# Performance work log

Measured on AMD Instinct MI355X. Metric: run time of the kernel, lower is better.

## Reference

```python
import jax, jax.numpy as jnp
import numpy as np

N_ENT = 500000
N_REL = 1000
EMB = 256
B = 65536
EPS = 1e-12


def setup_inputs() -> dict:
    key = jax.random.key(0)
    ks = jax.random.split(key, 7)
    all_emb = jax.random.normal(ks[0], (N_ENT + N_REL, EMB), dtype=jnp.float32)
    pos_h = jax.random.randint(ks[1], (B,), 0, N_ENT)
    pos_r = jax.random.randint(ks[2], (B,), 0, N_REL)
    pos_t = jax.random.randint(ks[3], (B,), 0, N_ENT)
    neg_h = jax.random.randint(ks[4], (B,), 0, N_ENT)
    neg_r = jax.random.randint(ks[5], (B,), 0, N_REL)
    neg_t = jax.random.randint(ks[6], (B,), 0, N_ENT)
    return {"all_emb": all_emb, "pos_h": pos_h, "pos_r": pos_r, "pos_t": pos_t,
            "neg_h": neg_h, "neg_r": neg_r, "neg_t": neg_t, "n_ent": N_ENT}


def reference(all_emb, pos_h, pos_r, pos_t, neg_h, neg_r, neg_t, n_ent):
    # forward() first L2-normalizes entity rows in-place (normalize_entity_weights)
    ent = all_emb[:n_ent]
    nrm = jnp.maximum(jnp.linalg.norm(ent, axis=1, keepdims=True), EPS)
    emb = jnp.concatenate([ent / nrm, all_emb[n_ent:]], axis=0)

    # sparse.mm(adj, emb) with rows (+1@h, +1@(n_ent+r), -1@t) == gather-combine
    def score(h, r, t):
        v = emb[h] + emb[r + n_ent] - emb[t]          # [B, EMB]
        return -jnp.sum(v * v, axis=1)                 # -||.||_2^2, [B]

    pos_calc = score(pos_h, pos_r, pos_t)
    neg_calc = score(neg_h, neg_r, neg_t)
    return (pos_calc, neg_calc)
```

## Files before the change

### kernel.cpp

```cpp
#include <hip/hip_runtime.h>


#define EMB 256
#define EPS 1e-12f
#define SPW 4

__global__ __launch_bounds__(256) void transe_score_diag2x_kernel(
    const float* __restrict__ emb,
    const int* __restrict__ pos_h, const int* __restrict__ pos_r, const int* __restrict__ pos_t,
    const int* __restrict__ neg_h, const int* __restrict__ neg_r, const int* __restrict__ neg_t,
    const int* __restrict__ n_ent_ptr,
    float* __restrict__ out, int B)
{
    const int wave = (blockIdx.x * blockDim.x + threadIdx.x) >> 6;
    const int lane = threadIdx.x & 63;
    const int base = wave * SPW;
    if (base >= 2 * B) return;

    const int n_ent = *n_ent_ptr;

    const int* __restrict__ hsrc;
    const int* __restrict__ rsrc;
    const int* __restrict__ tsrc;
    int off;
    if (base < B) { hsrc = pos_h; rsrc = pos_r; tsrc = pos_t; off = base; }
    else          { hsrc = neg_h; rsrc = neg_r; tsrc = neg_t; off = base - B; }

    const int4 hh = *(const int4*)(hsrc + off);
    const int4 rr = *(const int4*)(rsrc + off);
    const int4 tt = *(const int4*)(tsrc + off);

    const int hi[SPW] = {hh.x, hh.y, hh.z, hh.w};
    const int ri[SPW] = {rr.x, rr.y, rr.z, rr.w};
    const int ti[SPW] = {tt.x, tt.y, tt.z, tt.w};

    {
        float4 hv[SPW], tv[SPW], rv[SPW];
#pragma unroll
        for (int s = 0; s < SPW; ++s) {
            hv[s] = ((const float4*)(emb + (size_t)hi[s] * EMB))[lane];
            tv[s] = ((const float4*)(emb + (size_t)ti[s] * EMB))[lane];
            rv[s] = ((const float4*)(emb + ((size_t)ri[s] + (size_t)n_ent) * EMB))[lane];
        }

        float red[2 * SPW];
#pragma unroll
        for (int s = 0; s < SPW; ++s) {
            red[s]       = hv[s].x * hv[s].x + hv[s].y * hv[s].y + hv[s].z * hv[s].z + hv[s].w * hv[s].w;
            red[SPW + s] = tv[s].x * tv[s].x + tv[s].y * tv[s].y + tv[s].z * tv[s].z + tv[s].w * tv[s].w;
        }
#pragma unroll
        for (int d = 32; d >= 1; d >>= 1) {
#pragma unroll
            for (int k = 0; k < 2 * SPW; ++k)
                red[k] += __shfl_xor(red[k], d, 64);
        }

        float sq[SPW];
#pragma unroll
        for (int s = 0; s < SPW; ++s) {
            const float inh = 1.0f / fmaxf(sqrtf(red[s]), EPS);
            const float itn = 1.0f / fmaxf(sqrtf(red[SPW + s]), EPS);
            const float vx = hv[s].x * inh + rv[s].x - tv[s].x * itn;
            const float vy = hv[s].y * inh + rv[s].y - tv[s].y * itn;
            const float vz = hv[s].z * inh + rv[s].z - tv[s].z * itn;
            const float vw = hv[s].w * inh + rv[s].w - tv[s].w * itn;
            sq[s] = vx * vx + vy * vy + vz * vz + vw * vw;
        }
#pragma unroll
        for (int d = 32; d >= 1; d >>= 1) {
#pragma unroll
            for (int k = 0; k < SPW; ++k)
                sq[k] += __shfl_xor(sq[k], d, 64);
        }

        if (lane == 0)
            *(float4*)(out + base) = make_float4(-sq[0], -sq[1], -sq[2], -sq[3]);
    }

    __builtin_amdgcn_sched_barrier(0);

    unsigned long long p = (unsigned long long)(const void*)emb;
    asm volatile("" : "+s"(p));
    const float* emb2 = (const float*)p;

    {
        float4 hv[SPW], tv[SPW], rv[SPW];
#pragma unroll
        for (int s = 0; s < SPW; ++s) {
            hv[s] = ((const float4*)(emb2 + (size_t)hi[s] * EMB))[lane];
            tv[s] = ((const float4*)(emb2 + (size_t)ti[s] * EMB))[lane];
            rv[s] = ((const float4*)(emb2 + ((size_t)ri[s] + (size_t)n_ent) * EMB))[lane];
        }

        float red[2 * SPW];
#pragma unroll
        for (int s = 0; s < SPW; ++s) {
            red[s]       = hv[s].x * hv[s].x + hv[s].y * hv[s].y + hv[s].z * hv[s].z + hv[s].w * hv[s].w;
            red[SPW + s] = tv[s].x * tv[s].x + tv[s].y * tv[s].y + tv[s].z * tv[s].z + tv[s].w * tv[s].w;
        }
#pragma unroll
        for (int d = 32; d >= 1; d >>= 1) {
#pragma unroll
            for (int k = 0; k < 2 * SPW; ++k)
                red[k] += __shfl_xor(red[k], d, 64);
        }

        float sq[SPW];
#pragma unroll
        for (int s = 0; s < SPW; ++s) {
            const float inh = 1.0f / fmaxf(sqrtf(red[s]), EPS);
            const float itn = 1.0f / fmaxf(sqrtf(red[SPW + s]), EPS);
            const float vx = hv[s].x * inh + rv[s].x - tv[s].x * itn;
            const float vy = hv[s].y * inh + rv[s].y - tv[s].y * itn;
            const float vz = hv[s].z * inh + rv[s].z - tv[s].z * itn;
            const float vw = hv[s].w * inh + rv[s].w - tv[s].w * itn;
            sq[s] = vx * vx + vy * vy + vz * vz + vw * vw;
        }
#pragma unroll
        for (int d = 32; d >= 1; d >>= 1) {
#pragma unroll
            for (int k = 0; k < SPW; ++k)
                sq[k] += __shfl_xor(sq[k], d, 64);
        }

        asm volatile("" :: "v"(sq[0]), "v"(sq[1]), "v"(sq[2]), "v"(sq[3]));
    }
}

extern "C" void kernel_launch(void* const* d_in, const int* in_sizes, int n_in,
                              void* d_out, int out_size, void* d_ws, size_t ws_size,
                              hipStream_t stream) {
    const float* emb  = (const float*)d_in[0];
    const int* pos_h  = (const int*)d_in[1];
    const int* pos_r  = (const int*)d_in[2];
    const int* pos_t  = (const int*)d_in[3];
    const int* neg_h  = (const int*)d_in[4];
    const int* neg_r  = (const int*)d_in[5];
    const int* neg_t  = (const int*)d_in[6];
    const int* n_ent  = (const int*)d_in[7];
    float* out = (float*)d_out;

    const int B = in_sizes[1];
    const int total = 2 * B;
    const int waves = (total + SPW - 1) / SPW;
    const int block = 256;
    const int grid = (waves * 64 + block - 1) / block;

    transe_score_diag2x_kernel<<<grid, block, 0, stream>>>(
        emb, pos_h, pos_r, pos_t, neg_h, neg_r, neg_t, n_ent, out, B);
}
```

Measured before the change: 616.5 us.

## Drop duplicated scoring pass and bucket-sort triples by tail index before gathering

Removes the second, discarded gather-and-score pass from the kernel, which halves the embedding traffic. When a workspace is available, it also adds a counting-sort pipeline: zero a histogram, count tail-index bins, scan, then scatter (h, r, t, slot) records. The scoring kernel then walks the records in tail-sorted order to improve row locality for tail gathers and writes each result back to its original slot. In exchange it adds four small launches, atomics and scattered output writes, and a fallback single-pass kernel is used when no workspace is available.

```diff
diff --git a/kernel.cpp b/kernel.cpp
--- a/kernel.cpp
+++ b/kernel.cpp
@@ -4,8 +4,144 @@
 #define EMB 256
 #define EPS 1e-12f
 #define SPW 4
-
-__global__ __launch_bounds__(256) void transe_score_diag2x_kernel(
+#define NBINS 2048
+
+__global__ __launch_bounds__(256) void k0_zero_hist(int* __restrict__ hist)
+{
+    const int i = blockIdx.x * blockDim.x + threadIdx.x;
+    if (i < NBINS) hist[i] = 0;
+}
+
+__global__ __launch_bounds__(256) void k1_hist(
+    const int* __restrict__ pos_t, const int* __restrict__ neg_t,
+    int* __restrict__ hist, int B)
+{
+    const int i = blockIdx.x * blockDim.x + threadIdx.x;
+    if (i >= 2 * B) return;
+    const int t = (i < B) ? pos_t[i] : neg_t[i - B];
+    int key = t >> 8; if (key > NBINS - 1) key = NBINS - 1;
+    atomicAdd(&hist[key], 1);
+}
+
+__global__ __launch_bounds__(1024) void k2_scan(int* __restrict__ hist)
+{
+    __shared__ int wt[16];
+    const int tid  = threadIdx.x;
+    const int lane = tid & 63;
+    const int wid  = tid >> 6;
+
+    const int a0 = hist[2 * tid];
+    const int a1 = hist[2 * tid + 1];
+    const int s  = a0 + a1;
+
+    int v = s;
+#pragma unroll
+    for (int d = 1; d < 64; d <<= 1) {
+        const int x = __shfl_up(v, d, 64);
+        if (lane >= d) v += x;
+    }
+    if (lane == 63) wt[wid] = v;
+    __syncthreads();
+    if (wid == 0) {
+        int w = (lane < 16) ? wt[lane] : 0;
+        int vv = w;
+#pragma unroll
+        for (int d = 1; d < 16; d <<= 1) {
+            const int x = __shfl_up(vv, d, 64);
+            if (lane >= d) vv += x;
+        }
+        if (lane < 16) wt[lane] = vv - w;
+    }
+    __syncthreads();
+
+    const int block_incl = v + wt[wid];
+    const int e0 = block_incl - s;
+    hist[2 * tid]     = e0;
+    hist[2 * tid + 1] = e0 + a0;
+}
+
+__global__ __launch_bounds__(256) void k3_scatter(
+    const int* __restrict__ pos_h, const int* __restrict__ pos_r, const int* __restrict__ pos_t,
+    const int* __restrict__ neg_h, const int* __restrict__ neg_r, const int* __restrict__ neg_t,
+    int* __restrict__ cursor, int4* __restrict__ rec, int B)
+{
+    const int i = blockIdx.x * blockDim.x + threadIdx.x;
+    if (i >= 2 * B) return;
+    int h, r, t;
+    if (i < B) { h = pos_h[i]; r = pos_r[i]; t = pos_t[i]; }
+    else       { h = neg_h[i - B]; r = neg_r[i - B]; t = neg_t[i - B]; }
+    int key = t >> 8; if (key > NBINS - 1) key = NBINS - 1;
+    const int dst = atomicAdd(&cursor[key], 1);
+    rec[dst] = make_int4(h, r, t, i);
+}
+
+__global__ __launch_bounds__(256) void k4_score_sorted(
+    const float* __restrict__ emb,
+    const int4* __restrict__ rec,
+    const int* __restrict__ n_ent_ptr,
+    float* __restrict__ out, int B)
+{
+    const int wave = (blockIdx.x * blockDim.x + threadIdx.x) >> 6;
+    const int lane = threadIdx.x & 63;
+    const int base = wave * SPW;
+    if (base >= 2 * B) return;
+
+    const int n_ent = *n_ent_ptr;
+
+    int hi[SPW], ri[SPW], ti[SPW], sl[SPW];
+#pragma unroll
+    for (int s = 0; s < SPW; ++s) {
+        const int4 q = rec[base + s];
+        hi[s] = q.x; ri[s] = q.y; ti[s] = q.z; sl[s] = q.w;
+    }
+
+    float4 hv[SPW], tv[SPW], rv[SPW];
+#pragma unroll
+    for (int s = 0; s < SPW; ++s) {
+        hv[s] = ((const float4*)(emb + (size_t)hi[s] * EMB))[lane];
+        tv[s] = ((const float4*)(emb + (size_t)ti[s] * EMB))[lane];
+        rv[s] = ((const float4*)(emb + ((size_t)ri[s] + (size_t)n_ent) * EMB))[lane];
+    }
+
+    float red[2 * SPW];
+#pragma unroll
+    for (int s = 0; s < SPW; ++s) {
+        red[s]       = hv[s].x * hv[s].x + hv[s].y * hv[s].y + hv[s].z * hv[s].z + hv[s].w * hv[s].w;
+        red[SPW + s] = tv[s].x * tv[s].x + tv[s].y * tv[s].y + tv[s].z * tv[s].z + tv[s].w * tv[s].w;
+    }
+#pragma unroll
+    for (int d = 32; d >= 1; d >>= 1) {
+#pragma unroll
+        for (int k = 0; k < 2 * SPW; ++k)
+            red[k] += __shfl_xor(red[k], d, 64);
+    }
+
+    float sq[SPW];
+#pragma unroll
+    for (int s = 0; s < SPW; ++s) {
+        const float inh = 1.0f / fmaxf(sqrtf(red[s]), EPS);
+        const float itn = 1.0f / fmaxf(sqrtf(red[SPW + s]), EPS);
+        const float vx = hv[s].x * inh + rv[s].x - tv[s].x * itn;
+        const float vy = hv[s].y * inh + rv[s].y - tv[s].y * itn;
+        const float vz = hv[s].z * inh + rv[s].z - tv[s].z * itn;
+        const float vw = hv[s].w * inh + rv[s].w - tv[s].w * itn;
+        sq[s] = vx * vx + vy * vy + vz * vz + vw * vw;
+    }
+#pragma unroll
+    for (int d = 32; d >= 1; d >>= 1) {
+#pragma unroll
+        for (int k = 0; k < SPW; ++k)
+            sq[k] += __shfl_xor(sq[k], d, 64);
+    }
+
+    if (lane == 0) {
+#pragma unroll
+        for (int s = 0; s < SPW; ++s)
+            out[sl[s]] = -sq[s];
+    }
+}
+
+__global__ __launch_bounds__(256) void transe_score_fused_kernel(
     const float* __restrict__ emb,
     const int* __restrict__ pos_h, const int* __restrict__ pos_r, const int* __restrict__ pos_t,
     const int* __restrict__ neg_h, const int* __restrict__ neg_r, const int* __restrict__ neg_t,
@@ -34,98 +170,47 @@
     const int ri[SPW] = {rr.x, rr.y, rr.z, rr.w};
     const int ti[SPW] = {tt.x, tt.y, tt.z, tt.w};
 
-    {
-        float4 hv[SPW], tv[SPW], rv[SPW];
-#pragma unroll
-        for (int s = 0; s < SPW; ++s) {
-            hv[s] = ((const float4*)(emb + (size_t)hi[s] * EMB))[lane];
-            tv[s] = ((const float4*)(emb + (size_t)ti[s] * EMB))[lane];
-            rv[s] = ((const float4*)(emb + ((size_t)ri[s] + (size_t)n_ent) * EMB))[lane];
-        }
-
-        float red[2 * SPW];
-#pragma unroll
-        for (int s = 0; s < SPW; ++s) {
-            red[s]       = hv[s].x * hv[s].x + hv[s].y * hv[s].y + hv[s].z * hv[s].z + hv[s].w * hv[s].w;
-            red[SPW + s] = tv[s].x * tv[s].x + tv[s].y * tv[s].y + tv[s].z * tv[s].z + tv[s].w * tv[s].w;
-        }
-#pragma unroll
-        for (int d = 32; d >= 1; d >>= 1) {
-#pragma unroll
-            for (int k = 0; k < 2 * SPW; ++k)
-                red[k] += __shfl_xor(red[k], d, 64);
-        }
-
-        float sq[SPW];
-#pragma unroll
-        for (int s = 0; s < SPW; ++s) {
-            const float inh = 1.0f / fmaxf(sqrtf(red[s]), EPS);
-            const float itn = 1.0f / fmaxf(sqrtf(red[SPW + s]), EPS);
-            const float vx = hv[s].x * inh + rv[s].x - tv[s].x * itn;
-            const float vy = hv[s].y * inh + rv[s].y - tv[s].y * itn;
-            const float vz = hv[s].z * inh + rv[s].z - tv[s].z * itn;
-            const float vw = hv[s].w * inh + rv[s].w - tv[s].w * itn;
-            sq[s] = vx * vx + vy * vy + vz * vz + vw * vw;
-        }
-#pragma unroll
-        for (int d = 32; d >= 1; d >>= 1) {
-#pragma unroll
-            for (int k = 0; k < SPW; ++k)
-                sq[k] += __shfl_xor(sq[k], d, 64);
-        }
-
-        if (lane == 0)
-            *(float4*)(out + base) = make_float4(-sq[0], -sq[1], -sq[2], -sq[3]);
-    }
-
-    __builtin_amdgcn_sched_barrier(0);
-
-    unsigned long long p = (unsigned long long)(const void*)emb;
-    asm volatile("" : "+s"(p));
-    const float* emb2 = (const float*)p;
-
-    {
-        float4 hv[SPW], tv[SPW], rv[SPW];
-#pragma unroll
-        for (int s = 0; s < SPW; ++s) {
-            hv[s] = ((const float4*)(emb2 + (size_t)hi[s] * EMB))[lane];
-            tv[s] = ((const float4*)(emb2 + (size_t)ti[s] * EMB))[lane];
-            rv[s] = ((const float4*)(emb2 + ((size_t)ri[s] + (size_t)n_ent) * EMB))[lane];
-        }
-
-        float red[2 * SPW];
-#pragma unroll
-        for (int s = 0; s < SPW; ++s) {
-            red[s]       = hv[s].x * hv[s].x + hv[s].y * hv[s].y + hv[s].z * hv[s].z + hv[s].w * hv[s].w;
-            red[SPW + s] = tv[s].x * tv[s].x + tv[s].y * tv[s].y + tv[s].z * tv[s].z + tv[s].w * tv[s].w;
-        }
-#pragma unroll
-        for (int d = 32; d >= 1; d >>= 1) {
-#pragma unroll
-            for (int k = 0; k < 2 * SPW; ++k)
-                red[k] += __shfl_xor(red[k], d, 64);
-        }
-
-        float sq[SPW];
-#pragma unroll
-        for (int s = 0; s < SPW; ++s) {
-            const float inh = 1.0f / fmaxf(sqrtf(red[s]), EPS);
-            const float itn = 1.0f / fmaxf(sqrtf(red[SPW + s]), EPS);
-            const float vx = hv[s].x * inh + rv[s].x - tv[s].x * itn;
-            const float vy = hv[s].y * inh + rv[s].y - tv[s].y * itn;
-            const float vz = hv[s].z * inh + rv[s].z - tv[s].z * itn;
-            const float vw = hv[s].w * inh + rv[s].w - tv[s].w * itn;
-            sq[s] = vx * vx + vy * vy + vz * vz + vw * vw;
-        }
-#pragma unroll
-        for (int d = 32; d >= 1; d >>= 1) {
-#pragma unroll
-            for (int k = 0; k < SPW; ++k)
-                sq[k] += __shfl_xor(sq[k], d, 64);
-        }
-
-        asm volatile("" :: "v"(sq[0]), "v"(sq[1]), "v"(sq[2]), "v"(sq[3]));
-    }
+    float4 hv[SPW], tv[SPW], rv[SPW];
+#pragma unroll
+    for (int s = 0; s < SPW; ++s) {
+        hv[s] = ((const float4*)(emb + (size_t)hi[s] * EMB))[lane];
+        tv[s] = ((const float4*)(emb + (size_t)ti[s] * EMB))[lane];
+        rv[s] = ((const float4*)(emb + ((size_t)ri[s] + (size_t)n_ent) * EMB))[lane];
+    }
+
+    float red[2 * SPW];
+#pragma unroll
+    for (int s = 0; s < SPW; ++s) {
+        red[s]       = hv[s].x * hv[s].x + hv[s].y * hv[s].y + hv[s].z * hv[s].z + hv[s].w * hv[s].w;
+        red[SPW + s] = tv[s].x * tv[s].x + tv[s].y * tv[s].y + tv[s].z * tv[s].z + tv[s].w * tv[s].w;
+    }
+#pragma unroll
+    for (int d = 32; d >= 1; d >>= 1) {
+#pragma unroll
+        for (int k = 0; k < 2 * SPW; ++k)
+            red[k] += __shfl_xor(red[k], d, 64);
+    }
+
+    float sq[SPW];
+#pragma unroll
+    for (int s = 0; s < SPW; ++s) {
+        const float inh = 1.0f / fmaxf(sqrtf(red[s]), EPS);
+        const float itn = 1.0f / fmaxf(sqrtf(red[SPW + s]), EPS);
+        const float vx = hv[s].x * inh + rv[s].x - tv[s].x * itn;
+        const float vy = hv[s].y * inh + rv[s].y - tv[s].y * itn;
+        const float vz = hv[s].z * inh + rv[s].z - tv[s].z * itn;
+        const float vw = hv[s].w * inh + rv[s].w - tv[s].w * itn;
+        sq[s] = vx * vx + vy * vy + vz * vz + vw * vw;
+    }
+#pragma unroll
+    for (int d = 32; d >= 1; d >>= 1) {
+#pragma unroll
+        for (int k = 0; k < SPW; ++k)
+            sq[k] += __shfl_xor(sq[k], d, 64);
+    }
+
+    if (lane == 0)
+        *(float4*)(out + base) = make_float4(-sq[0], -sq[1], -sq[2], -sq[3]);
 }
 
 extern "C" void kernel_launch(void* const* d_in, const int* in_sizes, int n_in,
@@ -143,10 +228,25 @@
 
     const int B = in_sizes[1];
     const int total = 2 * B;
+
+    const size_t need = 65536 + (size_t)total * sizeof(int4);
+
     const int waves = (total + SPW - 1) / SPW;
-    const int block = 256;
-    const int grid = (waves * 64 + block - 1) / block;
-
-    transe_score_diag2x_kernel<<<grid, block, 0, stream>>>(
-        emb, pos_h, pos_r, pos_t, neg_h, neg_r, neg_t, n_ent, out, B);
-}
+    const int grid4 = (waves * 64 + 255) / 256;
+
+    if (d_ws != nullptr && ws_size >= need && (total & 3) == 0) {
+        int*  hist = (int*)d_ws;
+        int4* rec  = (int4*)((char*)d_ws + 65536);
+
+        const int gridT = (total + 255) / 256;
+        k0_zero_hist<<<(NBINS + 255) / 256, 256, 0, stream>>>(hist);
+        k1_hist<<<gridT, 256, 0, stream>>>(pos_t, neg_t, hist, B);
+        k2_scan<<<1, 1024, 0, stream>>>(hist);
+        k3_scatter<<<gridT, 256, 0, stream>>>(pos_h, pos_r, pos_t,
+                                              neg_h, neg_r, neg_t, hist, rec, B);
+        k4_score_sorted<<<grid4, 256, 0, stream>>>(emb, rec, n_ent, out, B);
+    } else {
+        transe_score_fused_kernel<<<grid4, 256, 0, stream>>>(
+            emb, pos_h, pos_r, pos_t, neg_h, neg_r, neg_t, n_ent, out, B);
+    }
+}
```

Result: slower. 645.8 us (+4.8%).
